# Kernel tuning notes

Hardware: AMD Instinct MI355X
Metric: run time of the kernel (lower is better)

The kernel has to match this reference:

```python
import jax, jax.numpy as jnp
import numpy as np

D_K = 64


def setup_inputs() -> dict:
    key = jax.random.key(0)
    kq, kk, kv = jax.random.split(key, 3)
    B, H, S, D = 4, 16, 2048, 64
    return {
        "query": jax.random.normal(kq, (B, H, S, D), dtype=jnp.float32),
        "key": jax.random.normal(kk, (B, H, S, D), dtype=jnp.float32),
        "value": jax.random.normal(kv, (B, H, S, D), dtype=jnp.float32),
        "to_mask": 1,
    }


def reference(query, key, value, to_mask):
    # QK^T / sqrt(d_k): [B,H,S,S]
    scores = jnp.einsum("bhqd,bhkd->bhqk", query, key) / jnp.sqrt(
        jnp.asarray(D_K, dtype=query.dtype)
    )
    if to_mask:
        S = scores.shape[-1]
        # upper-triangular (strictly above diagonal) gets large negative bias
        causal = jnp.triu(jnp.ones((S, S), dtype=scores.dtype), k=1)
        scores = scores + causal[None, None, :, :] * jnp.asarray(-1e19, scores.dtype)
    attn = jax.nn.softmax(scores, axis=-1)
    return jnp.einsum("bhqk,bhkd->bhqd", attn, value)
```

## Files before the change

kernel.cpp:

```cpp
#include <hip/hip_runtime.h>
#include <math.h>

#define S_LEN 2048
#define D_HEAD 64
#define NT 32
#define BM 128
#define BN 64
#define NQT (S_LEN / BM)
#define TILE_HALFS 4096
#define PSTRIDE 72
#define QSCALE (0.125f * 1.44269504088896340736f)

typedef _Float16 f16;
typedef f16 f16x4 __attribute__((ext_vector_type(4)));
typedef f16 f16x8 __attribute__((ext_vector_type(8)));
typedef float f32x4 __attribute__((ext_vector_type(4)));
typedef int i32x2 __attribute__((ext_vector_type(2)));
typedef int i32x4 __attribute__((ext_vector_type(4)));

#define ASYNC16(g, l)                                                          \
    __builtin_amdgcn_global_load_lds(                                          \
        (const __attribute__((address_space(1))) void*)(g),                    \
        (__attribute__((address_space(3))) void*)(l), 16, 0, 0)

__global__ __launch_bounds__(256)
void prepass_kernel(const float* __restrict__ K, const float* __restrict__ V,
                    f16* __restrict__ Kw, f16* __restrict__ Vw) {
    const int kt = blockIdx.x, bh = blockIdx.y, tid = threadIdx.x;
    const int t = tid >> 6, lane = tid & 63, c = lane & 15, quad = lane >> 4;
    const size_t gbase = (size_t)bh * S_LEN * D_HEAD + (size_t)kt * BN * D_HEAD;
    const size_t tb = ((size_t)bh * NT + kt) * TILE_HALFS;

    __shared__ float Vt_s[64][65];

    float4 vv[4];
    #pragma unroll
    for (int i = 0; i < 4; ++i) {
        const int fi = tid + i * 256;
        const int row = fi >> 4, d0 = (fi & 15) * 4;
        vv[i] = *(const float4*)(V + gbase + row * 64 + d0);
    }

    #pragma unroll
    for (int ch = 0; ch < 2; ++ch) {
        const float* src = K + gbase + (size_t)(t * 16 + c) * 64 + ch * 32 + quad * 8;
        const float4 a = *(const float4*)src;
        const float4 b = *(const float4*)(src + 4);
        f16 h[8];
        h[0] = (f16)a.x; h[1] = (f16)a.y; h[2] = (f16)a.z; h[3] = (f16)a.w;
        h[4] = (f16)b.x; h[5] = (f16)b.y; h[6] = (f16)b.z; h[7] = (f16)b.w;
        *(f16x8*)&Kw[tb + (size_t)((t * 2 + ch) * 64 + lane) * 8] = *(f16x8*)h;
    }

    #pragma unroll
    for (int i = 0; i < 4; ++i) {
        const int fi = tid + i * 256;
        const int row = fi >> 4, d0 = (fi & 15) * 4;
        Vt_s[row][d0 + 0] = vv[i].x; Vt_s[row][d0 + 1] = vv[i].y;
        Vt_s[row][d0 + 2] = vv[i].z; Vt_s[row][d0 + 3] = vv[i].w;
    }
    __syncthreads();
    #pragma unroll
    for (int ch = 0; ch < 2; ++ch) {
        f16 h[8];
        #pragma unroll
        for (int j = 0; j < 8; ++j)
            h[j] = (f16)Vt_s[ch * 32 + quad * 8 + j][t * 16 + c];
        *(f16x8*)&Vw[tb + (size_t)((t * 2 + ch) * 64 + lane) * 8] = *(f16x8*)h;
    }
}

__global__ __launch_bounds__(256, 4)
void fa_fwd_kernel(const float* __restrict__ Q, const f16* __restrict__ Kw,
                   const f16* __restrict__ Vw, const int* __restrict__ to_mask,
                   float* __restrict__ O) {
    const int linear = (int)blockIdx.x;
    const int g      = linear >> 3;
    const int qt     = (NQT - 1) - (g >> 3);
    const int bh     = (linear & 7) + 8 * (g & 7);

    const int tid  = threadIdx.x;
    const int wave = tid >> 6;
    const int lane = tid & 63;
    const int c    = lane & 15;
    const int quad = lane >> 4;
    const int i0   = qt * BM;
    const int wrow0 = i0 + wave * 32;

    const int mask_on = to_mask[0];
    const int kt_end  = mask_on ? (2 * qt + 1) : (NT - 1);

    __shared__ __align__(16) f16 KV[2][2][TILE_HALFS];

    const size_t base  = (size_t)bh * S_LEN * D_HEAD;
    const size_t tbase = (size_t)bh * NT * TILE_HALFS;

    f16x8 aq[2][2];
    #pragma unroll
    for (int set = 0; set < 2; ++set) {
        const float* qp = Q + base + (size_t)(wrow0 + set * 16 + c) * D_HEAD + quad * 8;
        #pragma unroll
        for (int ch = 0; ch < 2; ++ch) {
            const float4 a = *(const float4*)(qp + ch * 32);
            const float4 b = *(const float4*)(qp + ch * 32 + 4);
            aq[set][ch][0] = (f16)(a.x * QSCALE); aq[set][ch][1] = (f16)(a.y * QSCALE);
            aq[set][ch][2] = (f16)(a.z * QSCALE); aq[set][ch][3] = (f16)(a.w * QSCALE);
            aq[set][ch][4] = (f16)(b.x * QSCALE); aq[set][ch][5] = (f16)(b.y * QSCALE);
            aq[set][ch][6] = (f16)(b.z * QSCALE); aq[set][ch][7] = (f16)(b.w * QSCALE);
        }
    }

    f32x4 o[2][4];
    f32x4 accl[2];
    #pragma unroll
    for (int set = 0; set < 2; ++set) {
        accl[set] = (f32x4){0.f, 0.f, 0.f, 0.f};
        #pragma unroll
        for (int nt = 0; nt < 4; ++nt) o[set][nt] = (f32x4){0.f, 0.f, 0.f, 0.f};
    }

    const f16 one1 = (f16)1.0f;
    const f16x8 ones = {one1, one1, one1, one1, one1, one1, one1, one1};

    const int srcA = c + 32 * (quad & 1);
    const int srcB = srcA + 16;
    const bool rsel = (quad >> 1) != 0;

    asm volatile("s_waitcnt vmcnt(0)" ::: "memory");

    #pragma unroll
    for (int i = 0; i < 2; ++i) {
        const int s = wave * 2 + i;
        ASYNC16(Kw + tbase + s * 512 + lane * 8, &KV[0][0][s * 512]);
        ASYNC16(Vw + tbase + s * 512 + lane * 8, &KV[0][1][s * 512]);
    }
    #pragma unroll
    for (int i = 0; i < 2; ++i) {
        const int s = wave * 2 + i;
        ASYNC16(Kw + tbase + TILE_HALFS + s * 512 + lane * 8, &KV[1][0][s * 512]);
        ASYNC16(Vw + tbase + TILE_HALFS + s * 512 + lane * 8, &KV[1][1][s * 512]);
    }

    for (int kt = 0; kt <= kt_end; ++kt) {
        asm volatile("s_waitcnt vmcnt(4)" ::: "memory");
        __builtin_amdgcn_s_barrier();
        __builtin_amdgcn_sched_barrier(0);

        const int j0 = kt * BN;
        const f16* Kt = &KV[kt & 1][0][0];
        const f16* Vv = &KV[kt & 1][1][0];
        const bool active = !(mask_on && j0 > wrow0 + 31);

        if (active) {
            f32x4 s[2][4];
            #pragma unroll
            for (int t = 0; t < 4; ++t) {
                const f16x8 kf0 = *(const f16x8*)&Kt[(t * 2 + 0) * 512 + lane * 8];
                const f16x8 kf1 = *(const f16x8*)&Kt[(t * 2 + 1) * 512 + lane * 8];
                #pragma unroll
                for (int set = 0; set < 2; ++set) {
                    f32x4 acc = (f32x4){0.f, 0.f, 0.f, 0.f};
                    acc = __builtin_amdgcn_mfma_f32_16x16x32_f16(kf0, aq[set][0], acc, 0, 0, 0);
                    acc = __builtin_amdgcn_mfma_f32_16x16x32_f16(kf1, aq[set][1], acc, 0, 0, 0);
                    s[set][t] = acc;
                }
            }

            if (mask_on && j0 + 63 > wrow0) {
                #pragma unroll
                for (int set = 0; set < 2; ++set)
                    #pragma unroll
                    for (int t = 0; t < 4; ++t)
                        #pragma unroll
                        for (int r = 0; r < 4; ++r)
                            if (j0 + t * 16 + quad * 4 + r > wrow0 + set * 16 + c)
                                s[set][t][r] = -1e30f;
            }

            i32x2 pw[2][4];
            #pragma unroll
            for (int set = 0; set < 2; ++set)
                #pragma unroll
                for (int t2 = 0; t2 < 4; ++t2) {
                    f16x4 p;
                    #pragma unroll
                    for (int r = 0; r < 4; ++r)
                        p[r] = (f16)__builtin_amdgcn_exp2f(fminf(s[set][t2][r], 15.0f));
                    pw[set][t2] = *(i32x2*)&p;
                }

            f16x8 ap[2][2];
            #pragma unroll
            for (int set = 0; set < 2; ++set)
                #pragma unroll
                for (int h = 0; h < 2; ++h) {
                    const int w0x = pw[set][2 * h].x,     w0y = pw[set][2 * h].y;
                    const int w1x = pw[set][2 * h + 1].x, w1y = pw[set][2 * h + 1].y;
                    const int ax0 = __shfl(w0x, srcA, 64), ax1 = __shfl(w1x, srcA, 64);
                    const int ay0 = __shfl(w0y, srcA, 64), ay1 = __shfl(w1y, srcA, 64);
                    const int bx0 = __shfl(w0x, srcB, 64), bx1 = __shfl(w1x, srcB, 64);
                    const int by0 = __shfl(w0y, srcB, 64), by1 = __shfl(w1y, srcB, 64);
                    i32x4 packed;
                    packed.x = rsel ? ax1 : ax0;
                    packed.y = rsel ? ay1 : ay0;
                    packed.z = rsel ? bx1 : bx0;
                    packed.w = rsel ? by1 : by0;
                    ap[set][h] = *(f16x8*)&packed;
                }

            #pragma unroll
            for (int set = 0; set < 2; ++set) {
                accl[set] = __builtin_amdgcn_mfma_f32_16x16x32_f16(ap[set][0], ones, accl[set], 0, 0, 0);
                accl[set] = __builtin_amdgcn_mfma_f32_16x16x32_f16(ap[set][1], ones, accl[set], 0, 0, 0);
            }

            #pragma unroll
            for (int nt = 0; nt < 4; ++nt) {
                const f16x8 bv0 = *(const f16x8*)&Vv[(nt * 2 + 0) * 512 + lane * 8];
                const f16x8 bv1 = *(const f16x8*)&Vv[(nt * 2 + 1) * 512 + lane * 8];
                #pragma unroll
                for (int set = 0; set < 2; ++set) {
                    o[set][nt] = __builtin_amdgcn_mfma_f32_16x16x32_f16(ap[set][0], bv0, o[set][nt], 0, 0, 0);
                    o[set][nt] = __builtin_amdgcn_mfma_f32_16x16x32_f16(ap[set][1], bv1, o[set][nt], 0, 0, 0);
                }
            }
        }

        __builtin_amdgcn_s_barrier();
        __builtin_amdgcn_sched_barrier(0);

        {
            const int pf = (kt + 2 <= kt_end) ? (kt + 2) : kt_end;
            const size_t tb = tbase + (size_t)pf * TILE_HALFS;
            f16* lk = &KV[kt & 1][0][0];
            f16* lv = &KV[kt & 1][1][0];
            #pragma unroll
            for (int i = 0; i < 2; ++i) {
                const int s = wave * 2 + i;
                ASYNC16(Kw + tb + s * 512 + lane * 8, lk + s * 512);
                ASYNC16(Vw + tb + s * 512 + lane * 8, lv + s * 512);
            }
        }
    }

    asm volatile("s_waitcnt vmcnt(0)" ::: "memory");

    #pragma unroll
    for (int set = 0; set < 2; ++set)
        #pragma unroll
        for (int r = 0; r < 4; ++r) {
            const float inv = 1.0f / accl[set][r];
            float* op = O + base + (size_t)(wrow0 + set * 16 + quad * 4 + r) * D_HEAD;
            #pragma unroll
            for (int nt = 0; nt < 4; ++nt)
                op[nt * 16 + c] = o[set][nt][r] * inv;
        }
}

__global__ __launch_bounds__(256)
void fa_fwd_fallback(const float* __restrict__ Q, const float* __restrict__ K,
                     const float* __restrict__ V, const int* __restrict__ to_mask,
                     float* __restrict__ O) {
    const int qt = blockIdx.x, bh = blockIdx.y, tid = threadIdx.x;
    const int wave = tid >> 6, lane = tid & 63, c = lane & 15, quad = lane >> 4;
    const int i0 = qt * 64;
    const int mask_on = to_mask[0];
    const int kt_end = mask_on ? qt : (NT - 1);
    __shared__ __align__(16) f16 Ks[64][PSTRIDE];
    __shared__ __align__(16) f16 Vs[64][PSTRIDE];
    __shared__ __align__(16) f16 Psf[64][PSTRIDE];
    const size_t base = (size_t)bh * S_LEN * D_HEAD;
    f16x8 aq[2];
    {
        const float* qp = Q + base + (size_t)(i0 + wave * 16 + c) * D_HEAD + quad * 8;
        for (int ch = 0; ch < 2; ++ch)
            for (int j = 0; j < 8; ++j) aq[ch][j] = (f16)(qp[ch * 32 + j] * 0.125f);
    }
    f32x4 o[4]; float m_run[4], l_run[4], alpha_r[4];
    for (int t = 0; t < 4; ++t) o[t] = (f32x4){0.f, 0.f, 0.f, 0.f};
    for (int r = 0; r < 4; ++r) { m_run[r] = -INFINITY; l_run[r] = 0.f; }
    for (int kt = 0; kt <= kt_end; ++kt) {
        const int j0 = kt * 64;
        __syncthreads();
        for (int i = 0; i < 4; ++i) {
            const int f = tid + i * 256, key = f >> 4, d = (f & 15) * 4;
            const float4 kv = *(const float4*)(K + base + (size_t)(j0 + key) * D_HEAD + d);
            Ks[key][d] = (f16)kv.x; Ks[key][d + 1] = (f16)kv.y;
            Ks[key][d + 2] = (f16)kv.z; Ks[key][d + 3] = (f16)kv.w;
            const float4 vv = *(const float4*)(V + base + (size_t)(j0 + key) * D_HEAD + d);
            Vs[d][key] = (f16)vv.x; Vs[d + 1][key] = (f16)vv.y;
            Vs[d + 2][key] = (f16)vv.z; Vs[d + 3][key] = (f16)vv.w;
        }
        __syncthreads();
        f32x4 s[4];
        for (int t = 0; t < 4; ++t) {
            f32x4 acc = (f32x4){0.f, 0.f, 0.f, 0.f};
            const f16x8 b0 = *(const f16x8*)&Ks[t * 16 + c][quad * 8];
            const f16x8 b1 = *(const f16x8*)&Ks[t * 16 + c][32 + quad * 8];
            acc = __builtin_amdgcn_mfma_f32_16x16x32_f16(aq[0], b0, acc, 0, 0, 0);
            acc = __builtin_amdgcn_mfma_f32_16x16x32_f16(aq[1], b1, acc, 0, 0, 0);
            s[t] = acc;
        }
        if (mask_on && kt == qt)
            for (int t = 0; t < 4; ++t)
                for (int r = 0; r < 4; ++r)
                    if (t * 16 + c > wave * 16 + quad * 4 + r) s[t][r] = -1e30f;
        for (int r = 0; r < 4; ++r) {
            float mx = fmaxf(fmaxf(s[0][r], s[1][r]), fmaxf(s[2][r], s[3][r]));
            mx = fmaxf(mx, __shfl_xor(mx, 1)); mx = fmaxf(mx, __shfl_xor(mx, 2));
            mx = fmaxf(mx, __shfl_xor(mx, 4)); mx = fmaxf(mx, __shfl_xor(mx, 8));
            const float m_new = fmaxf(m_run[r], mx);
            const float alpha = __expf(m_run[r] - m_new);
            m_run[r] = m_new;
            float rs = 0.f;
            for (int t = 0; t < 4; ++t) { const float p = __expf(s[t][r] - m_new); s[t][r] = p; rs += p; }
            rs += __shfl_xor(rs, 1); rs += __shfl_xor(rs, 2);
            rs += __shfl_xor(rs, 4); rs += __shfl_xor(rs, 8);
            l_run[r] = l_run[r] * alpha + rs; alpha_r[r] = alpha;
        }
        for (int t = 0; t < 4; ++t)
            for (int r = 0; r < 4; ++r)
                Psf[wave * 16 + quad * 4 + r][t * 16 + c] = (f16)s[t][r];
        __syncthreads();
        const f16x8 ap0 = *(const f16x8*)&Psf[wave * 16 + c][quad * 8];
        const f16x8 ap1 = *(const f16x8*)&Psf[wave * 16 + c][32 + quad * 8];
        for (int t = 0; t < 4; ++t) {
            f32x4 acc = o[t];
            for (int r = 0; r < 4; ++r) acc[r] *= alpha_r[r];
            const f16x8 bv0 = *(const f16x8*)&Vs[t * 16 + c][quad * 8];
            const f16x8 bv1 = *(const f16x8*)&Vs[t * 16 + c][32 + quad * 8];
            acc = __builtin_amdgcn_mfma_f32_16x16x32_f16(ap0, bv0, acc, 0, 0, 0);
            acc = __builtin_amdgcn_mfma_f32_16x16x32_f16(ap1, bv1, acc, 0, 0, 0);
            o[t] = acc;
        }
    }
    for (int r = 0; r < 4; ++r) {
        const float inv = 1.f / l_run[r];
        float* op = O + base + (size_t)(i0 + wave * 16 + quad * 4 + r) * D_HEAD;
        for (int t = 0; t < 4; ++t) op[t * 16 + c] = o[t][r] * inv;
    }
}

extern "C" void kernel_launch(void* const* d_in, const int* in_sizes, int n_in,
                              void* d_out, int out_size, void* d_ws, size_t ws_size,
                              hipStream_t stream) {
    const float* Q = (const float*)d_in[0];
    const float* K = (const float*)d_in[1];
    const float* V = (const float*)d_in[2];
    const int* to_mask = (const int*)d_in[3];
    float* O = (float*)d_out;

    const size_t half_elems = (size_t)64 * S_LEN * D_HEAD;
    if (ws_size >= 2 * half_elems * sizeof(f16)) {
        f16* Kw = (f16*)d_ws;
        f16* Vw = Kw + half_elems;
        prepass_kernel<<<dim3(NT, 64), dim3(256), 0, stream>>>(K, V, Kw, Vw);
        fa_fwd_kernel<<<dim3(NQT * 64), dim3(256), 0, stream>>>(Q, Kw, Vw, to_mask, O);
    } else {
        fa_fwd_fallback<<<dim3(NT, 64), dim3(256), 0, stream>>>(Q, K, V, to_mask, O);
    }
}
```

Measured before the change: 186.9 us.

## Double query tile to 256 rows with 8 waves and triple-buffered K/V pipeline

Query tile per block doubles to 256 rows using 512 threads (8 waves), so each K/V tile loaded into LDS is shared by twice as many rows. The K/V ring grows to three LDS buffers, and the next prefetch is issued right after the barrier, before compute, so only one barrier per iteration is needed. Fully masked tiles are now skipped with continue. Block ordering is changed to interleave heavy and light causal tiles. The trade-off is half as many blocks, larger LDS per block, and more load imbalance across the causal triangle.

```diff
diff --git a/kernel.cpp b/kernel.cpp
--- a/kernel.cpp
+++ b/kernel.cpp
@@ -4,7 +4,7 @@
 #define S_LEN 2048
 #define D_HEAD 64
 #define NT 32
-#define BM 128
+#define BM 256
 #define BN 64
 #define NQT (S_LEN / BM)
 #define TILE_HALFS 4096
@@ -70,13 +70,14 @@
     }
 }
 
-__global__ __launch_bounds__(256, 4)
+__global__ __launch_bounds__(512, 4)
 void fa_fwd_kernel(const float* __restrict__ Q, const f16* __restrict__ Kw,
                    const f16* __restrict__ Vw, const int* __restrict__ to_mask,
                    float* __restrict__ O) {
     const int linear = (int)blockIdx.x;
     const int g      = linear >> 3;
-    const int qt     = (NQT - 1) - (g >> 3);
+    const int idx    = g >> 3;
+    const int qt     = (idx < 4) ? (7 - idx) : (idx - 4);
     const int bh     = (linear & 7) + 8 * (g & 7);
 
     const int tid  = threadIdx.x;
@@ -88,9 +89,9 @@
     const int wrow0 = i0 + wave * 32;
 
     const int mask_on = to_mask[0];
-    const int kt_end  = mask_on ? (2 * qt + 1) : (NT - 1);
-
-    __shared__ __align__(16) f16 KV[2][2][TILE_HALFS];
+    const int kt_end  = mask_on ? (4 * qt + 3) : (NT - 1);
+
+    __shared__ __align__(16) f16 KV[3][2][TILE_HALFS];
 
     const size_t base  = (size_t)bh * S_LEN * D_HEAD;
     const size_t tbase = (size_t)bh * NT * TILE_HALFS;
@@ -128,117 +129,101 @@
 
     asm volatile("s_waitcnt vmcnt(0)" ::: "memory");
 
-    #pragma unroll
-    for (int i = 0; i < 2; ++i) {
-        const int s = wave * 2 + i;
-        ASYNC16(Kw + tbase + s * 512 + lane * 8, &KV[0][0][s * 512]);
-        ASYNC16(Vw + tbase + s * 512 + lane * 8, &KV[0][1][s * 512]);
-    }
-    #pragma unroll
-    for (int i = 0; i < 2; ++i) {
-        const int s = wave * 2 + i;
-        ASYNC16(Kw + tbase + TILE_HALFS + s * 512 + lane * 8, &KV[1][0][s * 512]);
-        ASYNC16(Vw + tbase + TILE_HALFS + s * 512 + lane * 8, &KV[1][1][s * 512]);
-    }
+    ASYNC16(Kw + tbase + wave * 512 + lane * 8, &KV[0][0][wave * 512]);
+    ASYNC16(Vw + tbase + wave * 512 + lane * 8, &KV[0][1][wave * 512]);
+    ASYNC16(Kw + tbase + TILE_HALFS + wave * 512 + lane * 8, &KV[1][0][wave * 512]);
+    ASYNC16(Vw + tbase + TILE_HALFS + wave * 512 + lane * 8, &KV[1][1][wave * 512]);
 
     for (int kt = 0; kt <= kt_end; ++kt) {
-        asm volatile("s_waitcnt vmcnt(4)" ::: "memory");
-        __builtin_amdgcn_s_barrier();
-        __builtin_amdgcn_sched_barrier(0);
-
-        const int j0 = kt * BN;
-        const f16* Kt = &KV[kt & 1][0][0];
-        const f16* Vv = &KV[kt & 1][1][0];
-        const bool active = !(mask_on && j0 > wrow0 + 31);
-
-        if (active) {
-            f32x4 s[2][4];
-            #pragma unroll
-            for (int t = 0; t < 4; ++t) {
-                const f16x8 kf0 = *(const f16x8*)&Kt[(t * 2 + 0) * 512 + lane * 8];
-                const f16x8 kf1 = *(const f16x8*)&Kt[(t * 2 + 1) * 512 + lane * 8];
-                #pragma unroll
-                for (int set = 0; set < 2; ++set) {
-                    f32x4 acc = (f32x4){0.f, 0.f, 0.f, 0.f};
-                    acc = __builtin_amdgcn_mfma_f32_16x16x32_f16(kf0, aq[set][0], acc, 0, 0, 0);
-                    acc = __builtin_amdgcn_mfma_f32_16x16x32_f16(kf1, aq[set][1], acc, 0, 0, 0);
-                    s[set][t] = acc;
-                }
-            }
-
-            if (mask_on && j0 + 63 > wrow0) {
-                #pragma unroll
-                for (int set = 0; set < 2; ++set)
-                    #pragma unroll
-                    for (int t = 0; t < 4; ++t)
-                        #pragma unroll
-                        for (int r = 0; r < 4; ++r)
-                            if (j0 + t * 16 + quad * 4 + r > wrow0 + set * 16 + c)
-                                s[set][t][r] = -1e30f;
-            }
-
-            i32x2 pw[2][4];
-            #pragma unroll
-            for (int set = 0; set < 2; ++set)
-                #pragma unroll
-                for (int t2 = 0; t2 < 4; ++t2) {
-                    f16x4 p;
-                    #pragma unroll
-                    for (int r = 0; r < 4; ++r)
-                        p[r] = (f16)__builtin_amdgcn_exp2f(fminf(s[set][t2][r], 15.0f));
-                    pw[set][t2] = *(i32x2*)&p;
-                }
-
-            f16x8 ap[2][2];
-            #pragma unroll
-            for (int set = 0; set < 2; ++set)
-                #pragma unroll
-                for (int h = 0; h < 2; ++h) {
-                    const int w0x = pw[set][2 * h].x,     w0y = pw[set][2 * h].y;
-                    const int w1x = pw[set][2 * h + 1].x, w1y = pw[set][2 * h + 1].y;
-                    const int ax0 = __shfl(w0x, srcA, 64), ax1 = __shfl(w1x, srcA, 64);
-                    const int ay0 = __shfl(w0y, srcA, 64), ay1 = __shfl(w1y, srcA, 64);
-                    const int bx0 = __shfl(w0x, srcB, 64), bx1 = __shfl(w1x, srcB, 64);
-                    const int by0 = __shfl(w0y, srcB, 64), by1 = __shfl(w1y, srcB, 64);
-                    i32x4 packed;
-                    packed.x = rsel ? ax1 : ax0;
-                    packed.y = rsel ? ay1 : ay0;
-                    packed.z = rsel ? bx1 : bx0;
-                    packed.w = rsel ? by1 : by0;
-                    ap[set][h] = *(f16x8*)&packed;
-                }
-
-            #pragma unroll
-            for (int set = 0; set < 2; ++set) {
-                accl[set] = __builtin_amdgcn_mfma_f32_16x16x32_f16(ap[set][0], ones, accl[set], 0, 0, 0);
-                accl[set] = __builtin_amdgcn_mfma_f32_16x16x32_f16(ap[set][1], ones, accl[set], 0, 0, 0);
-            }
-
-            #pragma unroll
-            for (int nt = 0; nt < 4; ++nt) {
-                const f16x8 bv0 = *(const f16x8*)&Vv[(nt * 2 + 0) * 512 + lane * 8];
-                const f16x8 bv1 = *(const f16x8*)&Vv[(nt * 2 + 1) * 512 + lane * 8];
-                #pragma unroll
-                for (int set = 0; set < 2; ++set) {
-                    o[set][nt] = __builtin_amdgcn_mfma_f32_16x16x32_f16(ap[set][0], bv0, o[set][nt], 0, 0, 0);
-                    o[set][nt] = __builtin_amdgcn_mfma_f32_16x16x32_f16(ap[set][1], bv1, o[set][nt], 0, 0, 0);
-                }
-            }
-        }
-
+        asm volatile("s_waitcnt vmcnt(2)" ::: "memory");
         __builtin_amdgcn_s_barrier();
         __builtin_amdgcn_sched_barrier(0);
 
         {
             const int pf = (kt + 2 <= kt_end) ? (kt + 2) : kt_end;
             const size_t tb = tbase + (size_t)pf * TILE_HALFS;
-            f16* lk = &KV[kt & 1][0][0];
-            f16* lv = &KV[kt & 1][1][0];
-            #pragma unroll
-            for (int i = 0; i < 2; ++i) {
-                const int s = wave * 2 + i;
-                ASYNC16(Kw + tb + s * 512 + lane * 8, lk + s * 512);
-                ASYNC16(Vw + tb + s * 512 + lane * 8, lv + s * 512);
+            f16* lk = &KV[(kt + 2) % 3][0][0];
+            f16* lv = &KV[(kt + 2) % 3][1][0];
+            ASYNC16(Kw + tb + wave * 512 + lane * 8, lk + wave * 512);
+            ASYNC16(Vw + tb + wave * 512 + lane * 8, lv + wave * 512);
+        }
+
+        const int j0 = kt * BN;
+        if (mask_on && j0 > wrow0 + 31) continue;
+
+        const f16* Kt = &KV[kt % 3][0][0];
+        const f16* Vv = &KV[kt % 3][1][0];
+
+        f32x4 s[2][4];
+        #pragma unroll
+        for (int t = 0; t < 4; ++t) {
+            const f16x8 kf0 = *(const f16x8*)&Kt[(t * 2 + 0) * 512 + lane * 8];
+            const f16x8 kf1 = *(const f16x8*)&Kt[(t * 2 + 1) * 512 + lane * 8];
+            #pragma unroll
+            for (int set = 0; set < 2; ++set) {
+                f32x4 acc = (f32x4){0.f, 0.f, 0.f, 0.f};
+                acc = __builtin_amdgcn_mfma_f32_16x16x32_f16(kf0, aq[set][0], acc, 0, 0, 0);
+                acc = __builtin_amdgcn_mfma_f32_16x16x32_f16(kf1, aq[set][1], acc, 0, 0, 0);
+                s[set][t] = acc;
+            }
+        }
+
+        if (mask_on && j0 + 63 > wrow0) {
+            #pragma unroll
+            for (int set = 0; set < 2; ++set)
+                #pragma unroll
+                for (int t = 0; t < 4; ++t)
+                    #pragma unroll
+                    for (int r = 0; r < 4; ++r)
+                        if (j0 + t * 16 + quad * 4 + r > wrow0 + set * 16 + c)
+                            s[set][t][r] = -1e30f;
+        }
+
+        i32x2 pw[2][4];
+        #pragma unroll
+        for (int set = 0; set < 2; ++set)
+            #pragma unroll
+            for (int t2 = 0; t2 < 4; ++t2) {
+                f16x4 p;
+                #pragma unroll
+                for (int r = 0; r < 4; ++r)
+                    p[r] = (f16)__builtin_amdgcn_exp2f(fminf(s[set][t2][r], 15.0f));
+                pw[set][t2] = *(i32x2*)&p;
+            }
+
+        f16x8 ap[2][2];
+        #pragma unroll
+        for (int set = 0; set < 2; ++set)
+            #pragma unroll
+            for (int h = 0; h < 2; ++h) {
+                const int w0x = pw[set][2 * h].x,     w0y = pw[set][2 * h].y;
+                const int w1x = pw[set][2 * h + 1].x, w1y = pw[set][2 * h + 1].y;
+                const int ax0 = __shfl(w0x, srcA, 64), ax1 = __shfl(w1x, srcA, 64);
+                const int ay0 = __shfl(w0y, srcA, 64), ay1 = __shfl(w1y, srcA, 64);
+                const int bx0 = __shfl(w0x, srcB, 64), bx1 = __shfl(w1x, srcB, 64);
+                const int by0 = __shfl(w0y, srcB, 64), by1 = __shfl(w1y, srcB, 64);
+                i32x4 packed;
+                packed.x = rsel ? ax1 : ax0;
+                packed.y = rsel ? ay1 : ay0;
+                packed.z = rsel ? bx1 : bx0;
+                packed.w = rsel ? by1 : by0;
+                ap[set][h] = *(f16x8*)&packed;
+            }
+
+        #pragma unroll
+        for (int set = 0; set < 2; ++set) {
+            accl[set] = __builtin_amdgcn_mfma_f32_16x16x32_f16(ap[set][0], ones, accl[set], 0, 0, 0);
+            accl[set] = __builtin_amdgcn_mfma_f32_16x16x32_f16(ap[set][1], ones, accl[set], 0, 0, 0);
+        }
+
+        #pragma unroll
+        for (int nt = 0; nt < 4; ++nt) {
+            const f16x8 bv0 = *(const f16x8*)&Vv[(nt * 2 + 0) * 512 + lane * 8];
+            const f16x8 bv1 = *(const f16x8*)&Vv[(nt * 2 + 1) * 512 + lane * 8];
+            #pragma unroll
+            for (int set = 0; set < 2; ++set) {
+                o[set][nt] = __builtin_amdgcn_mfma_f32_16x16x32_f16(ap[set][0], bv0, o[set][nt], 0, 0, 0);
+                o[set][nt] = __builtin_amdgcn_mfma_f32_16x16x32_f16(ap[set][1], bv1, o[set][nt], 0, 0, 0);
             }
         }
     }
@@ -355,7 +340,7 @@
         f16* Kw = (f16*)d_ws;
         f16* Vw = Kw + half_elems;
         prepass_kernel<<<dim3(NT, 64), dim3(256), 0, stream>>>(K, V, Kw, Vw);
-        fa_fwd_kernel<<<dim3(NQT * 64), dim3(256), 0, stream>>>(Q, Kw, Vw, to_mask, O);
+        fa_fwd_kernel<<<dim3(NQT * 64), dim3(512), 0, stream>>>(Q, Kw, Vw, to_mask, O);
     } else {
         fa_fwd_fallback<<<dim3(NT, 64), dim3(256), 0, stream>>>(Q, K, V, to_mask, O);
     }
```

After: 187.1 us. About the same (+0.1%).
